# Optimization experiments

Measured on AMD Instinct MI355X. Metric: run time of the kernel, lower is better.

The kernel has to match this reference:

```python
import jax, jax.numpy as jnp
import numpy as np

BITS = 4
MAXQ = (1 << BITS) - 1  # 15
PACK = 32 // BITS       # 8 nibbles per int32


def setup_inputs() -> dict:
    key = jax.random.key(0)
    k = jax.random.split(key, 6)
    B, S, IN, OUT, G = 4, 2048, 4096, 4096, 32
    groups = IN // G  # 128
    imin, imax = np.iinfo(np.int32).min, np.iinfo(np.int32).max
    x = jax.random.normal(k[0], (B, S, IN), dtype=jnp.float32)
    qweight = jax.random.randint(k[1], (IN // PACK, OUT), imin, imax, dtype=jnp.int32)
    qzeros = jax.random.randint(k[2], (groups, OUT // PACK), imin, imax, dtype=jnp.int32)
    qscales = jax.random.randint(k[3], (groups, OUT, 1), 0, 256, dtype=jnp.int32)
    qscales_zeros = jax.random.uniform(k[4], (groups, 1, 1), dtype=jnp.float32)
    qscales_scales = jax.random.uniform(k[5], (groups, 1, 1), dtype=jnp.float32) * 0.01
    g_idx = (jnp.arange(IN, dtype=jnp.int32) // G)
    return {"x": x, "qweight": qweight, "qzeros": qzeros, "qscales": qscales,
            "qscales_zeros": qscales_zeros, "qscales_scales": qscales_scales, "g_idx": g_idx}


def reference(x, qweight, qzeros, qscales, qscales_zeros, qscales_scales, g_idx):
    out_features = qweight.shape[-1]
    shifts = jnp.arange(0, 32, BITS, dtype=jnp.int32)  # (8,)
    # --- unpack int4 weights: (in/8, 8, out) -> (in, out); mask makes arith shift == logical
    w = (qweight[:, None, :] >> shifts[None, :, None]) & MAXQ
    w = w.reshape(-1, out_features)  # (in, out), values 0..15
    # --- unpack zeros: (groups, out/8, 8) -> (groups, out); +1 per original
    z = ((qzeros[:, :, None] >> shifts[None, None, :]) & MAXQ) + 1
    z = z.reshape(qzeros.shape[0], -1)  # (groups, out)
    z = z[g_idx]  # (in, out)
    # --- double-dequant scales: (groups, out, 1) with (groups, 1, 1) stats
    scales = (qscales.astype(x.dtype) - qscales_zeros) * qscales_scales
    scales = scales.reshape(qscales.shape[0], -1)[g_idx]  # (in, out)
    weight = ((w - z) * scales).astype(x.dtype)  # (in, out)
    return jnp.matmul(x, weight)
```

## Files before the change

kernel.cpp:

```cpp
#include <hip/hip_runtime.h>

typedef __attribute__((ext_vector_type(8))) short short8;
typedef __attribute__((ext_vector_type(4))) float floatx4;
typedef unsigned int u32;
typedef unsigned short u16;

__device__ __forceinline__ u16 f2bf(float f) {
  u32 u = __float_as_uint(f);
  u += 0x7FFFu + ((u >> 16) & 1u);
  return (u16)(u >> 16);
}

typedef const __attribute__((address_space(1))) u32* gp1_t;
typedef __attribute__((address_space(3))) u32* lp3_t;

__device__ __forceinline__ void gld16(const void* g, void* l) {
  __builtin_amdgcn_global_load_lds((gp1_t)g, (lp3_t)l, 16, 0, 0);
}

__global__ __launch_bounds__(256) void xconv(const float* __restrict__ x,
                                             u16* __restrict__ xb, long long n4) {
  long long i = (long long)blockIdx.x * 256 + threadIdx.x;
  if (i >= n4) return;
  float4 v = ((const float4*)x)[i];
  ushort4 o;
  o.x = f2bf(v.x); o.y = f2bf(v.y); o.z = f2bf(v.z); o.w = f2bf(v.w);
  ((ushort4*)xb)[i] = o;
}

__global__ __launch_bounds__(256) void dequant(
    const int* __restrict__ qw, const int* __restrict__ qz,
    const int* __restrict__ qs, const float* __restrict__ qsz,
    const float* __restrict__ qss, const int* __restrict__ gidx,
    u16* __restrict__ Wt, int IN, int OUT) {
  const int n = blockIdx.x * 64 + (threadIdx.x & 63);
  const int w = threadIdx.x >> 6;
  const int k0 = blockIdx.y * 128 + w * 32;
  const int g = gidx[k0];
  const int kk0 = k0 >> 3;
  const int zq = ((qz[(size_t)g * (OUT >> 3) + (n >> 3)] >> (4 * (n & 7))) & 15) + 1;
  const float sc = ((float)qs[(size_t)g * OUT + n] - qsz[g]) * qss[g];
  u16* dst = Wt + (size_t)n * IN + k0;
#pragma unroll
  for (int j = 0; j < 4; ++j) {
    const int w32 = qw[(size_t)(kk0 + j) * OUT + n];
    u16 o[8];
#pragma unroll
    for (int s = 0; s < 8; ++s)
      o[s] = f2bf((float)(((w32 >> (4 * s)) & 15) - zq) * sc);
    uint4 pk;
    pk.x = (u32)o[0] | ((u32)o[1] << 16);
    pk.y = (u32)o[2] | ((u32)o[3] << 16);
    pk.z = (u32)o[4] | ((u32)o[5] << 16);
    pk.w = (u32)o[6] | ((u32)o[7] << 16);
    *(uint4*)(dst + j * 8) = pk;
  }
}

__global__ __launch_bounds__(256) void gemm(const u16* __restrict__ A,
                                            const u16* __restrict__ Bt,
                                            float* __restrict__ C,
                                            int M, int N, int K) {
  __shared__ u16 As[128 * 64];
  __shared__ u16 Bs[128 * 64];
  const int tid = threadIdx.x;
  const int lane = tid & 63;
  const int wave = tid >> 6;
  const int wm = wave & 1, wn = wave >> 1;
  const int lr = lane & 15, quad = lane >> 4;
  const int m0 = blockIdx.y * 128, n0 = blockIdx.x * 128;

  floatx4 acc[4][4] = {};

  const int srowB = (lane >> 3);
  const int schunk = (lane & 7) ^ srowB;
  const int rowA0 = wave * 32;
  const u16* aSrc = A + (size_t)(m0 + rowA0 + srowB) * K + schunk * 8;
  const u16* bSrc = Bt + (size_t)(n0 + rowA0 + srowB) * K + schunk * 8;
  u16* aDst = &As[rowA0 * 64];
  u16* bDst = &Bs[rowA0 * 64];
  const size_t rstep = (size_t)8 * K;

  const int rx = lr & 7;

  for (int k0 = 0; k0 < K; k0 += 64) {
    __syncthreads();
#pragma unroll
    for (int c = 0; c < 4; ++c) {
      gld16(aSrc + c * rstep + k0, aDst + c * 8 * 64);
      gld16(bSrc + c * rstep + k0, bDst + c * 8 * 64);
    }
    __syncthreads();

#pragma unroll
    for (int h = 0; h < 2; ++h) {
      short8 aF[4], bF[4];
      const int rc = ((quad + 4 * h) ^ rx) * 8;
#pragma unroll
      for (int t = 0; t < 4; ++t) {
        aF[t] = *(const short8*)&As[(wm * 64 + t * 16 + lr) * 64 + rc];
        bF[t] = *(const short8*)&Bs[(wn * 64 + t * 16 + lr) * 64 + rc];
      }
#pragma unroll
      for (int mt = 0; mt < 4; ++mt)
#pragma unroll
        for (int nt = 0; nt < 4; ++nt)
          acc[mt][nt] = __builtin_amdgcn_mfma_f32_16x16x32_bf16(
              aF[mt], bF[nt], acc[mt][nt], 0, 0, 0);
    }
  }

#pragma unroll
  for (int mt = 0; mt < 4; ++mt)
#pragma unroll
    for (int nt = 0; nt < 4; ++nt)
#pragma unroll
      for (int r = 0; r < 4; ++r) {
        int row = m0 + wm * 64 + mt * 16 + quad * 4 + r;
        int col = n0 + wn * 64 + nt * 16 + lr;
        C[(size_t)row * N + col] = acc[mt][nt][r];
      }
}

__global__ void naive(const float* __restrict__ x, const int* __restrict__ qw,
                      const int* __restrict__ qz, const int* __restrict__ qs,
                      const float* __restrict__ qsz, const float* __restrict__ qss,
                      const int* __restrict__ gidx, float* __restrict__ out,
                      int M, int N, int K) {
  int n = blockIdx.x * 64 + (threadIdx.x & 63);
  int m = blockIdx.y * 4 + (threadIdx.x >> 6);
  if (n >= N || m >= M) return;
  float acc = 0.f;
  for (int kk = 0; kk < K / 8; ++kk) {
    int w32 = qw[(size_t)kk * N + n];
#pragma unroll
    for (int s = 0; s < 8; ++s) {
      int k = kk * 8 + s;
      int g = gidx[k];
      int zq = ((qz[(size_t)g * (N >> 3) + (n >> 3)] >> (4 * (n & 7))) & 15) + 1;
      float sc = ((float)qs[(size_t)g * N + n] - qsz[g]) * qss[g];
      acc += x[(size_t)m * K + k] * ((float)((w32 >> (4 * s)) & 15) - (float)zq) * sc;
    }
  }
  out[(size_t)m * N + n] = acc;
}

extern "C" void kernel_launch(void* const* d_in, const int* in_sizes, int n_in,
                              void* d_out, int out_size, void* d_ws, size_t ws_size,
                              hipStream_t stream) {
  const float* x = (const float*)d_in[0];
  const int* qw = (const int*)d_in[1];
  const int* qz = (const int*)d_in[2];
  const int* qs = (const int*)d_in[3];
  const float* qsz = (const float*)d_in[4];
  const float* qss = (const float*)d_in[5];
  const int* gidx = (const int*)d_in[6];
  const int IN = in_sizes[6];
  const int OUT = (int)(((long long)in_sizes[1] * 8) / IN);
  const int M = in_sizes[0] / IN;
  float* out = (float*)d_out;

  size_t bytesW = (size_t)IN * OUT * 2;
  size_t bytesX = (size_t)M * IN * 2;
  bool fast = (ws_size >= bytesW + bytesX) && (M % 128 == 0) && (OUT % 128 == 0) &&
              (IN % 128 == 0) && ((size_t)M * IN % 4 == 0);

  if (fast) {
    u16* Wt = (u16*)d_ws;
    u16* Xb = (u16*)((char*)d_ws + bytesW);
    long long n4 = (long long)M * IN / 4;
    int cb = (int)((n4 + 255) / 256);
    xconv<<<cb, 256, 0, stream>>>(x, Xb, n4);
    dequant<<<dim3(OUT / 64, IN / 128), 256, 0, stream>>>(qw, qz, qs, qsz, qss,
                                                          gidx, Wt, IN, OUT);
    gemm<<<dim3(OUT / 128, M / 128), 256, 0, stream>>>(Xb, Wt, out, M, OUT, IN);
  } else {
    naive<<<dim3((OUT + 63) / 64, (M + 3) / 4), 256, 0, stream>>>(
        x, qw, qz, qs, qsz, qss, gidx, out, M, OUT, IN);
  }
}
```

Measured before the change: 547.1 us.

## Add 256x256 tiled GEMM with 4-stage LDS ring pipeline and XCD-aware block swizzle

Adds a new 512-thread GEMM kernel with 256x256 output tiles and a 4-deep shared-memory ring buffer. Global-to-LDS loads for stage s+3 are issued while MFMAs run on stage s, with explicit vmcnt waits, barriers and raised wave priority around the MFMA blocks. Workgroup IDs are remapped so consecutive tiles land on the same XCD, improving L2 reuse. The larger tile raises arithmetic intensity and hides memory latency, but uses more registers and LDS per block and depends on hand-counted waitcnt values being correct.

```diff
diff --git a/kernel.cpp b/kernel.cpp
--- a/kernel.cpp
+++ b/kernel.cpp
@@ -55,6 +55,119 @@
     pk.w = (u32)o[6] | ((u32)o[7] << 16);
     *(uint4*)(dst + j * 8) = pk;
   }
+}
+
+__global__ __launch_bounds__(512, 2) void gemm256(const u16* __restrict__ A,
+                                                  const u16* __restrict__ Bt,
+                                                  float* __restrict__ C,
+                                                  int M, int N, int K) {
+  __shared__ u16 As[4][256 * 32];
+  __shared__ u16 Bs[4][256 * 32];
+  const int tid = threadIdx.x;
+  const int lane = tid & 63;
+  const int wave = tid >> 6;
+  const int wm = wave >> 2;
+  const int wn = wave & 3;
+  const int lr = lane & 15, quad = lane >> 4;
+
+  const int nbx = N >> 8;
+  const int nwg = gridDim.x;
+  const int bid = blockIdx.x;
+  const int q8 = nwg >> 3, r8 = nwg & 7;
+  const int xcd = bid & 7, loc = bid >> 3;
+  const int swz = (xcd < r8 ? xcd * (q8 + 1) : r8 * (q8 + 1) + (xcd - r8) * q8) + loc;
+  const int n0 = (swz % nbx) << 8;
+  const int m0 = (swz / nbx) << 8;
+
+  floatx4 acc[8][4] = {};
+
+  const int schunk = (lane & 3) ^ ((lane >> 3) & 3);
+  const u16* aS = A + (size_t)(m0 + wave * 16 + (lane >> 2)) * K + schunk * 8;
+  const u16* bS = Bt + (size_t)(n0 + wave * 16 + (lane >> 2)) * K + schunk * 8;
+  const size_t cstep = (size_t)128 * K;
+
+  const int rx = (quad ^ ((lr >> 1) & 3)) * 8;
+  const int abase = (wm * 128 + lr) * 32 + rx;
+  const int bbase = (wn * 64 + lr) * 32 + rx;
+
+  const int NS = K >> 5;
+
+  for (int s = 0; s < 3; ++s) {
+    const u16* ga = aS + (size_t)s * 32;
+    const u16* gb = bS + (size_t)s * 32;
+    gld16(ga, &As[s][wave * 512]);
+    gld16(ga + cstep, &As[s][wave * 512 + 4096]);
+    gld16(gb, &Bs[s][wave * 512]);
+    gld16(gb + cstep, &Bs[s][wave * 512 + 4096]);
+  }
+  asm volatile("s_waitcnt vmcnt(8)" ::: "memory");
+  __builtin_amdgcn_s_barrier();
+
+#define GSTEP(sv, DO_STAGE, VMW)                                               \
+  do {                                                                         \
+    const int ring_ = (sv) & 3;                                                \
+    const u16* pa_ = &As[ring_][abase];                                        \
+    const u16* pb_ = &Bs[ring_][bbase];                                        \
+        \
+    if (DO_STAGE) {                                                            \
+      const int r2_ = ((sv) + 3) & 3;                                          \
+      const u16* ga_ = aS + (size_t)((sv) + 3) * 32;                           \
+      gld16(ga_, &As[r2_][wave * 512]);                                        \
+      gld16(ga_ + cstep, &As[r2_][wave * 512 + 4096]);                         \
+    }                                                                          \
+    short8 aF[4], bF[4];                                                       \
+    _Pragma("unroll") for (int t = 0; t < 4; ++t)                              \
+        aF[t] = *(const short8*)(pa_ + t * 512);                               \
+    _Pragma("unroll") for (int t = 0; t < 4; ++t)                              \
+        bF[t] = *(const short8*)(pb_ + t * 512);                               \
+    __builtin_amdgcn_s_barrier();                                              \
+    __builtin_amdgcn_s_setprio(1);                                             \
+    _Pragma("unroll") for (int mt = 0; mt < 4; ++mt)                           \
+      _Pragma("unroll") for (int nt = 0; nt < 4; ++nt)                         \
+        acc[mt][nt] = __builtin_amdgcn_mfma_f32_16x16x32_bf16(                 \
+            aF[mt], bF[nt], acc[mt][nt], 0, 0, 0);                             \
+    __builtin_amdgcn_s_setprio(0);                                             \
+    __builtin_amdgcn_s_barrier();                                              \
+        \
+    if (DO_STAGE) {                                                            \
+      const int r2_ = ((sv) + 3) & 3;                                          \
+      const u16* gb_ = bS + (size_t)((sv) + 3) * 32;                           \
+      gld16(gb_, &Bs[r2_][wave * 512]);                                        \
+      gld16(gb_ + cstep, &Bs[r2_][wave * 512 + 4096]);                         \
+    }                                                                          \
+    _Pragma("unroll") for (int t = 0; t < 4; ++t)                              \
+        aF[t] = *(const short8*)(pa_ + 2048 + t * 512);                        \
+    __builtin_amdgcn_s_setprio(1);                                             \
+    _Pragma("unroll") for (int mt = 0; mt < 4; ++mt)                           \
+      _Pragma("unroll") for (int nt = 0; nt < 4; ++nt)                         \
+        acc[4 + mt][nt] = __builtin_amdgcn_mfma_f32_16x16x32_bf16(             \
+            aF[mt], bF[nt], acc[4 + mt][nt], 0, 0, 0);                         \
+    __builtin_amdgcn_s_setprio(0);                                             \
+    VMW;                                                                       \
+    __builtin_amdgcn_s_barrier();                                              \
+  } while (0)
+
+  int s = 0;
+  const int NSm3 = NS - 3;
+  for (; s < NSm3; ++s)
+    GSTEP(s, 1, asm volatile("s_waitcnt vmcnt(8)" ::: "memory"));
+  GSTEP(s, 0, asm volatile("s_waitcnt vmcnt(4)" ::: "memory")); ++s;
+  GSTEP(s, 0, asm volatile("s_waitcnt vmcnt(0)" ::: "memory")); ++s;
+  GSTEP(s, 0, (void)0);
+#undef GSTEP
+
+#pragma unroll
+  for (int qm = 0; qm < 2; ++qm)
+#pragma unroll
+    for (int mt = 0; mt < 4; ++mt)
+#pragma unroll
+      for (int nt = 0; nt < 4; ++nt)
+#pragma unroll
+        for (int r = 0; r < 4; ++r) {
+          int row = m0 + wm * 128 + qm * 64 + mt * 16 + quad * 4 + r;
+          int col = n0 + wn * 64 + nt * 16 + lr;
+          C[(size_t)row * N + col] = acc[qm * 4 + mt][nt][r];
+        }
 }
 
 __global__ __launch_bounds__(256) void gemm(const u16* __restrict__ A,
@@ -162,10 +275,11 @@
 
   size_t bytesW = (size_t)IN * OUT * 2;
   size_t bytesX = (size_t)M * IN * 2;
-  bool fast = (ws_size >= bytesW + bytesX) && (M % 128 == 0) && (OUT % 128 == 0) &&
-              (IN % 128 == 0) && ((size_t)M * IN % 4 == 0);
-
-  if (fast) {
+  bool haveWs = (ws_size >= bytesW + bytesX);
+  bool fast256 = haveWs && (M % 256 == 0) && (OUT % 256 == 0) && (IN % 128 == 0);
+  bool fast128 = haveWs && (M % 128 == 0) && (OUT % 128 == 0) && (IN % 128 == 0);
+
+  if (fast256 || fast128) {
     u16* Wt = (u16*)d_ws;
     u16* Xb = (u16*)((char*)d_ws + bytesW);
     long long n4 = (long long)M * IN / 4;
@@ -173,7 +287,12 @@
     xconv<<<cb, 256, 0, stream>>>(x, Xb, n4);
     dequant<<<dim3(OUT / 64, IN / 128), 256, 0, stream>>>(qw, qz, qs, qsz, qss,
                                                           gidx, Wt, IN, OUT);
-    gemm<<<dim3(OUT / 128, M / 128), 256, 0, stream>>>(Xb, Wt, out, M, OUT, IN);
+    if (fast256) {
+      int nblk = (M / 256) * (OUT / 256);
+      gemm256<<<dim3(nblk), 512, 0, stream>>>(Xb, Wt, out, M, OUT, IN);
+    } else {
+      gemm<<<dim3(OUT / 128, M / 128), 256, 0, stream>>>(Xb, Wt, out, M, OUT, IN);
+    }
   } else {
     naive<<<dim3((OUT + 63) / 64, (M + 3) / 4), 256, 0, stream>>>(
         x, qw, qz, qs, qsz, qss, gidx, out, M, OUT, IN);
```

New measurement: 549.8 us. About the same (+0.5%).

## Add 256x256 double-buffered 8-wave GEMM with XCD swizzle and phased prefetch

Applied to the files above, without the earlier changes.

Adds a new GEMM kernel that computes 256x256 output tiles with 512 threads. It double-buffers LDS, issues asynchronous global-to-LDS loads interleaved with MFMA phases under explicit vmcnt waits and barriers, raises wave priority during MFMA, and remaps block IDs so neighbouring tiles land on the same XCD for better L2 reuse. The goal is to hide global load latency and raise arithmetic intensity compared with the single-buffered 128x128 kernel. In exchange it uses more LDS and registers, and the hand-written wait counts and barriers are fragile.

```diff
diff --git a/kernel.cpp b/kernel.cpp
--- a/kernel.cpp
+++ b/kernel.cpp
@@ -55,6 +55,120 @@
     pk.w = (u32)o[6] | ((u32)o[7] << 16);
     *(uint4*)(dst + j * 8) = pk;
   }
+}
+
+#define VM4 asm volatile("s_waitcnt vmcnt(4)" ::: "memory")
+#define VM0 asm volatile("s_waitcnt vmcnt(0)" ::: "memory")
+
+__global__ __launch_bounds__(512, 2) void gemm256(const u16* __restrict__ A,
+                                                  const u16* __restrict__ Bt,
+                                                  float* __restrict__ C,
+                                                  int M, int N, int K) {
+  __shared__ u16 As[2][16384];
+  __shared__ u16 Bs[2][16384];
+  const int tid = threadIdx.x;
+  const int lane = tid & 63;
+  const int wave = tid >> 6;
+  const int wm = wave >> 2;
+  const int wn = wave & 3;
+  const int lr = lane & 15, quad = lane >> 4;
+
+  const int nbx = N >> 8;
+  const int nwg = gridDim.x;
+  const int bid = blockIdx.x;
+  const int q8 = nwg >> 3, r8 = nwg & 7;
+  const int xcd = bid & 7, loc = bid >> 3;
+  const int swz = (xcd < r8 ? xcd * (q8 + 1) : r8 * (q8 + 1) + (xcd - r8) * q8) + loc;
+  const int n0 = (swz % nbx) << 8;
+  const int m0 = (swz / nbx) << 8;
+
+  floatx4 acc[8][4] = {};
+
+  const int srow = lane >> 3;
+  const int sch8 = ((lane & 7) ^ (srow & 7)) * 8;
+  const u16* aS = A + (size_t)(m0 + wave * 8 + srow) * K + sch8;
+  const u16* bS = Bt + (size_t)(n0 + wave * 8 + srow) * K + sch8;
+
+#define STAGE_A(buf, h, kt) do {                                              \
+    const u16* s_ = aS + (size_t)(h) * 128 * K + (size_t)(kt) * 64;           \
+    u16* d_ = &As[buf][((h) * 128 + wave * 8) * 64];                          \
+    gld16(s_, d_); gld16(s_ + (size_t)64 * K, d_ + 4096);                     \
+  } while (0)
+#define STAGE_B(buf, h, kt) do {                                              \
+    const u16* s_ = bS + (size_t)(h) * 128 * K + (size_t)(kt) * 64;           \
+    u16* d_ = &Bs[buf][((h) * 128 + wave * 8) * 64];                          \
+    gld16(s_, d_); gld16(s_ + (size_t)64 * K, d_ + 4096);                     \
+  } while (0)
+
+  const int rl = lr & 7;
+  const int cs0 = ((0 * 4 + quad) ^ rl) * 8;
+  const int cs1 = ((1 * 4 + quad) ^ rl) * 8;
+  const u16* a0rd = &As[0][(wm * 128 + lr) * 64];
+  const u16* a1rd = &As[1][(wm * 128 + lr) * 64];
+  const u16* b0rd = &Bs[0][(wn * 64 + lr) * 64];
+  const u16* b1rd = &Bs[1][(wn * 64 + lr) * 64];
+
+  short8 aF[2][2], bF[4][2];
+
+#define PHASE(ARD, BRD, q, LOADB, STG, VMW) do {                              \
+    if (LOADB) {                                                              \
+      _Pragma("unroll") for (int nt = 0; nt < 4; ++nt) {                      \
+        bF[nt][0] = *(const short8*)((BRD) + nt * 1024 + cs0);                \
+        bF[nt][1] = *(const short8*)((BRD) + nt * 1024 + cs1);                \
+      }                                                                       \
+    }                                                                         \
+    aF[0][0] = *(const short8*)((ARD) + (2 * (q)) * 1024 + cs0);              \
+    aF[0][1] = *(const short8*)((ARD) + (2 * (q)) * 1024 + cs1);              \
+    aF[1][0] = *(const short8*)((ARD) + (2 * (q) + 1) * 1024 + cs0);          \
+    aF[1][1] = *(const short8*)((ARD) + (2 * (q) + 1) * 1024 + cs1);          \
+    STG;                                                                      \
+    __builtin_amdgcn_s_barrier();                                             \
+    __builtin_amdgcn_s_setprio(1);                                            \
+    _Pragma("unroll") for (int s = 0; s < 2; ++s)                             \
+      _Pragma("unroll") for (int j = 0; j < 2; ++j)                           \
+        _Pragma("unroll") for (int nt = 0; nt < 4; ++nt)                      \
+          acc[2 * (q) + j][nt] = __builtin_amdgcn_mfma_f32_16x16x32_bf16(     \
+              aF[j][s], bF[nt][s], acc[2 * (q) + j][nt], 0, 0, 0);            \
+    __builtin_amdgcn_s_setprio(0);                                            \
+    VMW;                                                                      \
+    __builtin_amdgcn_s_barrier();                                             \
+  } while (0)
+
+  STAGE_B(0, 0, 0); STAGE_B(0, 1, 0);
+  STAGE_A(0, 0, 0); STAGE_A(0, 1, 0);
+  STAGE_B(1, 0, 1); STAGE_B(1, 1, 1);
+  VM4;
+  __builtin_amdgcn_s_barrier();
+
+  const int NI = K >> 7;
+  for (int i = 0; i < NI; ++i) {
+    const int kt = 2 * i;
+    const bool full = (i < NI - 1);
+    PHASE(a0rd, b0rd, 0, 1, { STAGE_A(1, 0, kt + 1); }, (void)0);
+    PHASE(a0rd, b0rd, 1, 0, { STAGE_A(1, 1, kt + 1); }, (void)0);
+    PHASE(a0rd, b0rd, 2, 0, { if (full) STAGE_B(0, 0, kt + 2); }, (void)0);
+    PHASE(a0rd, b0rd, 3, 0, { if (full) STAGE_B(0, 1, kt + 2); },
+          { if (full) { VM4; } else { VM0; } });
+    PHASE(a1rd, b1rd, 0, 1, { if (full) STAGE_A(0, 0, kt + 2); }, (void)0);
+    PHASE(a1rd, b1rd, 1, 0, { if (full) STAGE_A(0, 1, kt + 2); }, (void)0);
+    PHASE(a1rd, b1rd, 2, 0, { if (full) STAGE_B(1, 0, kt + 3); }, (void)0);
+    PHASE(a1rd, b1rd, 3, 0, { if (full) STAGE_B(1, 1, kt + 3); },
+          { if (full) { VM4; } });
+  }
+#undef PHASE
+#undef STAGE_A
+#undef STAGE_B
+
+#pragma unroll
+  for (int mt = 0; mt < 8; ++mt)
+#pragma unroll
+    for (int nt = 0; nt < 4; ++nt)
+#pragma unroll
+      for (int r = 0; r < 4; ++r) {
+        int row = m0 + wm * 128 + mt * 16 + quad * 4 + r;
+        int col = n0 + wn * 64 + nt * 16 + lr;
+        C[(size_t)row * N + col] = acc[mt][nt][r];
+      }
 }
 
 __global__ __launch_bounds__(256) void gemm(const u16* __restrict__ A,
@@ -162,10 +276,12 @@
 
   size_t bytesW = (size_t)IN * OUT * 2;
   size_t bytesX = (size_t)M * IN * 2;
-  bool fast = (ws_size >= bytesW + bytesX) && (M % 128 == 0) && (OUT % 128 == 0) &&
-              (IN % 128 == 0) && ((size_t)M * IN % 4 == 0);
-
-  if (fast) {
+  bool haveWs = (ws_size >= bytesW + bytesX);
+  bool fast256 = haveWs && (M % 256 == 0) && (OUT % 256 == 0) &&
+                 (IN % 128 == 0) && (IN >= 256);
+  bool fast128 = haveWs && (M % 128 == 0) && (OUT % 128 == 0) && (IN % 128 == 0);
+
+  if (fast256 || fast128) {
     u16* Wt = (u16*)d_ws;
     u16* Xb = (u16*)((char*)d_ws + bytesW);
     long long n4 = (long long)M * IN / 4;
@@ -173,7 +289,12 @@
     xconv<<<cb, 256, 0, stream>>>(x, Xb, n4);
     dequant<<<dim3(OUT / 64, IN / 128), 256, 0, stream>>>(qw, qz, qs, qsz, qss,
                                                           gidx, Wt, IN, OUT);
-    gemm<<<dim3(OUT / 128, M / 128), 256, 0, stream>>>(Xb, Wt, out, M, OUT, IN);
+    if (fast256) {
+      int nblk = (M / 256) * (OUT / 256);
+      gemm256<<<dim3(nblk), 512, 0, stream>>>(Xb, Wt, out, M, OUT, IN);
+    } else {
+      gemm<<<dim3(OUT / 128, M / 128), 256, 0, stream>>>(Xb, Wt, out, M, OUT, IN);
+    }
   } else {
     naive<<<dim3((OUT + 63) / 64, (M + 3) / 4), 256, 0, stream>>>(
         x, qw, qz, qs, qsz, qss, gidx, out, M, OUT, IN);
```

After: 489.8 us. 1.12x faster.
